# Performance work log

Hardware: AMD Instinct MI355X
Metric: run time of the kernel (lower is better)

## Reference

```python
import jax, jax.numpy as jnp
import numpy as np

LOG_SQRT_2PI = np.float32(0.5 * np.log(2.0 * np.pi))


def setup_inputs() -> dict:
    key = jax.random.key(0)
    k1, k2 = jax.random.split(key)
    B, M, K = 512, 256, 2
    z1 = jax.random.normal(k1, (B, 2 * M), dtype=jnp.float32)
    z2 = jax.random.normal(k2, (K * B, M), dtype=jnp.float32)
    return {"z1": z1, "z2": z2}


def reference(z1, z2):
    B = z1.shape[0]
    M = z2.shape[1]
    z1r = z1.reshape(B, 2, M)
    means = z1r[:, 0, :]                      # (B, M)
    stds = jnp.exp(z1r[:, 1, :] * 0.5)        # (B, M)
    z2r = z2.reshape(-1, B, M).transpose(1, 0, 2)  # (B, K, M)
    # Pairwise Normal log-prob: broadcast to (B_i, B_j, K, M)
    diff = (z2r[None, :, :, :] - means[:, None, None, :]) / stds[:, None, None, :]
    logp = -0.5 * diff * diff - jnp.log(stds)[:, None, None, :] - LOG_SQRT_2PI
    kernel = jnp.exp(logp).mean(axis=(2, 3))  # (B, B) likelihood kernel
    pos_sim = jnp.diagonal(kernel)
    return pos_sim.mean()
```

## Files before the change

### kernel.cpp

```cpp
#include <hip/hip_runtime.h>
#include <math.h>

#define PB 512
#define PM 256
#define PK 2

#define GRID1 128
#define I_PER_BLK (PB / GRID1)

#define SCALE (0.3989422804014327f / (512.0f * 512.0f))

__global__ __launch_bounds__(256)
void pp_partial(const float* __restrict__ z1,
                const float* __restrict__ z2,
                float* __restrict__ ws) {
    const int m = threadIdx.x;

    float acc = 0.0f;
    #pragma unroll
    for (int ii = 0; ii < I_PER_BLK; ++ii) {
        const int i = blockIdx.x * I_PER_BLK + ii;
        const float mean = z1[i * (2 * PM) + m];
        const float lv   = z1[i * (2 * PM) + PM + m];
        const float inv_std = __expf(-0.5f * lv);

        const float x0 = z2[(0 * PB + i) * PM + m];
        const float x1 = z2[(1 * PB + i) * PM + m];
        const float d0 = (x0 - mean) * inv_std;
        const float d1 = (x1 - mean) * inv_std;
        acc += (__expf(-0.5f * d0 * d0) + __expf(-0.5f * d1 * d1)) * inv_std;
    }

    #pragma unroll
    for (int off = 32; off > 0; off >>= 1)
        acc += __shfl_down(acc, off, 64);

    __shared__ float partial[4];
    const int wave = threadIdx.x >> 6;
    const int lane = threadIdx.x & 63;
    if (lane == 0) partial[wave] = acc;
    __syncthreads();

    if (threadIdx.x == 0)
        ws[blockIdx.x] = partial[0] + partial[1] + partial[2] + partial[3];
}

__global__ __launch_bounds__(64)
void pp_final(const float* __restrict__ ws, float* __restrict__ out) {
    const int lane = threadIdx.x;
    float v = ws[lane] + ws[lane + 64];
    #pragma unroll
    for (int off = 32; off > 0; off >>= 1)
        v += __shfl_down(v, off, 64);
    if (lane == 0) out[0] = v * SCALE;
}

extern "C" void kernel_launch(void* const* d_in, const int* in_sizes, int n_in,
                              void* d_out, int out_size, void* d_ws, size_t ws_size,
                              hipStream_t stream) {
    const float* z1 = (const float*)d_in[0];
    const float* z2 = (const float*)d_in[1];
    float* out = (float*)d_out;
    float* ws  = (float*)d_ws;

    pp_partial<<<GRID1, 256, 0, stream>>>(z1, z2, ws);
    pp_final<<<1, 64, 0, stream>>>(ws, out);
}
```

Baseline: 11.19 us.

## Fuse partial and final reductions via cooperative grid sync with float4 row loads

Merges the two-kernel reduction into one cooperative kernel that uses a grid-wide sync before block 0 does the final sum, removing a second kernel launch. It also changes the work mapping so each wave handles one row and loads four elements per lane as float4, replacing scalar loads. Cooperative launch and grid sync add their own overhead and a launch-path cost that may offset the saved launch.

```diff
diff --git a/kernel.cpp b/kernel.cpp
--- a/kernel.cpp
+++ b/kernel.cpp
@@ -1,34 +1,51 @@
 #include <hip/hip_runtime.h>
+#include <hip/hip_cooperative_groups.h>
 #include <math.h>
+
+namespace cg = cooperative_groups;
 
 #define PB 512
 #define PM 256
-#define PK 2
 
 #define GRID1 128
-#define I_PER_BLK (PB / GRID1)
+#define ROWS_PER_BLK 4
 
 #define SCALE (0.3989422804014327f / (512.0f * 512.0f))
 
 __global__ __launch_bounds__(256)
-void pp_partial(const float* __restrict__ z1,
-                const float* __restrict__ z2,
-                float* __restrict__ ws) {
-    const int m = threadIdx.x;
+void pp_fused(const float* __restrict__ z1,
+              const float* __restrict__ z2,
+              float* __restrict__ ws,
+              float* __restrict__ out) {
+    const int wave = threadIdx.x >> 6;
+    const int lane = threadIdx.x & 63;
+    const int i = blockIdx.x * ROWS_PER_BLK + wave;
+
+    const float4 mean = ((const float4*)&z1[i * (2 * PM)])[lane];
+    const float4 lv   = ((const float4*)&z1[i * (2 * PM) + PM])[lane];
+    const float4 x0   = ((const float4*)&z2[i * PM])[lane];
+    const float4 x1   = ((const float4*)&z2[(PB + i) * PM])[lane];
 
     float acc = 0.0f;
-    #pragma unroll
-    for (int ii = 0; ii < I_PER_BLK; ++ii) {
-        const int i = blockIdx.x * I_PER_BLK + ii;
-        const float mean = z1[i * (2 * PM) + m];
-        const float lv   = z1[i * (2 * PM) + PM + m];
-        const float inv_std = __expf(-0.5f * lv);
-
-        const float x0 = z2[(0 * PB + i) * PM + m];
-        const float x1 = z2[(1 * PB + i) * PM + m];
-        const float d0 = (x0 - mean) * inv_std;
-        const float d1 = (x1 - mean) * inv_std;
-        acc += (__expf(-0.5f * d0 * d0) + __expf(-0.5f * d1 * d1)) * inv_std;
+    {
+        const float is = __expf(-0.5f * lv.x);
+        const float d0 = (x0.x - mean.x) * is, d1 = (x1.x - mean.x) * is;
+        acc += (__expf(-0.5f * d0 * d0) + __expf(-0.5f * d1 * d1)) * is;
+    }
+    {
+        const float is = __expf(-0.5f * lv.y);
+        const float d0 = (x0.y - mean.y) * is, d1 = (x1.y - mean.y) * is;
+        acc += (__expf(-0.5f * d0 * d0) + __expf(-0.5f * d1 * d1)) * is;
+    }
+    {
+        const float is = __expf(-0.5f * lv.z);
+        const float d0 = (x0.z - mean.z) * is, d1 = (x1.z - mean.z) * is;
+        acc += (__expf(-0.5f * d0 * d0) + __expf(-0.5f * d1 * d1)) * is;
+    }
+    {
+        const float is = __expf(-0.5f * lv.w);
+        const float d0 = (x0.w - mean.w) * is, d1 = (x1.w - mean.w) * is;
+        acc += (__expf(-0.5f * d0 * d0) + __expf(-0.5f * d1 * d1)) * is;
     }
 
     #pragma unroll
@@ -36,23 +53,20 @@
         acc += __shfl_down(acc, off, 64);
 
     __shared__ float partial[4];
-    const int wave = threadIdx.x >> 6;
-    const int lane = threadIdx.x & 63;
     if (lane == 0) partial[wave] = acc;
     __syncthreads();
-
     if (threadIdx.x == 0)
         ws[blockIdx.x] = partial[0] + partial[1] + partial[2] + partial[3];
-}
 
-__global__ __launch_bounds__(64)
-void pp_final(const float* __restrict__ ws, float* __restrict__ out) {
-    const int lane = threadIdx.x;
-    float v = ws[lane] + ws[lane + 64];
-    #pragma unroll
-    for (int off = 32; off > 0; off >>= 1)
-        v += __shfl_down(v, off, 64);
-    if (lane == 0) out[0] = v * SCALE;
+    cg::this_grid().sync();
+
+    if (blockIdx.x == 0 && threadIdx.x < 64) {
+        float v = ws[threadIdx.x] + ws[threadIdx.x + 64];
+        #pragma unroll
+        for (int off = 32; off > 0; off >>= 1)
+            v += __shfl_down(v, off, 64);
+        if (threadIdx.x == 0) out[0] = v * SCALE;
+    }
 }
 
 extern "C" void kernel_launch(void* const* d_in, const int* in_sizes, int n_in,
@@ -63,6 +77,7 @@
     float* out = (float*)d_out;
     float* ws  = (float*)d_ws;
 
-    pp_partial<<<GRID1, 256, 0, stream>>>(z1, z2, ws);
-    pp_final<<<1, 64, 0, stream>>>(ws, out);
+    void* args[] = { (void*)&z1, (void*)&z2, (void*)&ws, (void*)&out };
+    hipLaunchCooperativeKernel((void*)pp_fused, dim3(GRID1), dim3(256),
+                               args, 0, stream);
 }
```

After: 32.99 us. +194.8%, slower.
